# Performance work log

Measured on AMD Instinct MI355X. Metric: run time of the kernel, lower is better.

Reference implementation:

```python
import jax, jax.numpy as jnp
import numpy as np

L, B, D_IN, H, N, NUM_LAYERS = 2048, 16, 64, 512, 64, 4


def setup_inputs() -> dict:
    key = jax.random.key(0)
    ks = jax.random.split(key, 9)
    x = jax.random.normal(ks[0], (L, B, D_IN), dtype=jnp.float32)
    enc_W = jax.random.normal(ks[1], (D_IN, H), dtype=jnp.float32) / np.sqrt(D_IN)
    enc_b = jax.random.normal(ks[2], (H,), dtype=jnp.float32) * 0.01
    # Per-layer S4D parameters, stacked along leading layer axis.
    log_dt = jax.random.uniform(ks[3], (NUM_LAYERS, H), dtype=jnp.float32,
                                minval=np.log(1e-3), maxval=np.log(1e-1))
    log_A_re = jnp.log(0.5 * jnp.ones((NUM_LAYERS, H, N), dtype=jnp.float32))
    A_im = jnp.broadcast_to(np.pi * jnp.arange(N, dtype=jnp.float32),
                            (NUM_LAYERS, H, N)).copy()
    C_re = jax.random.normal(ks[4], (NUM_LAYERS, H, N), dtype=jnp.float32)
    C_im = jax.random.normal(ks[5], (NUM_LAYERS, H, N), dtype=jnp.float32)
    Dskip = jax.random.normal(ks[6], (NUM_LAYERS, H), dtype=jnp.float32)
    return {"x": x, "enc_W": enc_W, "enc_b": enc_b, "log_dt": log_dt,
            "log_A_re": log_A_re, "A_im": A_im, "C_re": C_re, "C_im": C_im,
            "Dskip": Dskip}


def _s4d_layer(u, log_dt, log_A_re, A_im, C_re, C_im, Dskip):
    """u: [L,B,H] real. Diagonal SSM recurrent scan (ZOH discretization)."""
    dt = jnp.exp(log_dt)[:, None]                      # [H,1]
    A = -jnp.exp(log_A_re) + 1j * A_im                 # [H,N] complex, Re<0
    dA = jnp.exp(dt * A)                               # [H,N]
    dB = (dA - 1.0) / A                                # [H,N]
    C = (C_re + 1j * C_im).astype(jnp.complex64)       # [H,N]

    def step(s, u_t):                                  # s:[B,H,N] c64, u_t:[B,H]
        s = dA * s + dB * u_t[..., None]
        y = 2.0 * jnp.einsum('hn,bhn->bh', C, s).real + Dskip * u_t
        return s, y.astype(u_t.dtype)

    s0 = jnp.zeros((u.shape[1], u.shape[2], A.shape[-1]), dtype=jnp.complex64)
    sT, ys = jax.lax.scan(step, s0, u)
    return ys, sT


def reference(x, enc_W, enc_b, log_dt, log_A_re, A_im, C_re, C_im, Dskip):
    # batch_first=False: x is [L,B,D_IN]; torch code transposes to [B,L,·],
    # applies encoder, runs layers, transposes back -> equivalent to keeping
    # time-major [L,B,H] throughout.
    h = x @ enc_W + enc_b                              # [L,B,H]
    states_re, states_im = [], []
    for i in range(NUM_LAYERS):
        h, sT = _s4d_layer(h, log_dt[i], log_A_re[i], A_im[i],
                           C_re[i], C_im[i], Dskip[i])
        states_re.append(sT.real)
        states_im.append(sT.imag)
    return h, jnp.stack(states_re), jnp.stack(states_im)
```

## Files before the change

kernel.cpp:

```cpp
#include <hip/hip_runtime.h>
#include <math.h>

#define L_SEQ 2048
#define B_SZ 16
#define DIN 64
#define H_SZ 512
#define N_ST 64
#define N_LAYERS 4
#define Q_CHUNK 64
#define N_CHUNKS (L_SEQ / Q_CHUNK)
#define GSZ 4
#define N_GROUPS (N_CHUNKS / GSZ)
#define UPAD 2056

typedef _Float16 f16;
typedef _Float16 f16x8 __attribute__((ext_vector_type(8)));
typedef _Float16 f16x4 __attribute__((ext_vector_type(4)));
typedef _Float16 f16x2 __attribute__((ext_vector_type(2)));
typedef float    f32x4 __attribute__((ext_vector_type(4)));
typedef float    f32x2 __attribute__((ext_vector_type(2)));

template <int CTRL>
__device__ __forceinline__ float dpp_add(float x) {
    int s = __builtin_amdgcn_update_dpp(0, __builtin_bit_cast(int, x), CTRL, 0xF, 0xF, false);
    return x + __builtin_bit_cast(float, s);
}
__device__ __forceinline__ float wave_sum_lane63(float x) {
    x = dpp_add<0x111>(x);
    x = dpp_add<0x112>(x);
    x = dpp_add<0x114>(x);
    x = dpp_add<0x118>(x);
    x = dpp_add<0x142>(x);
    x = dpp_add<0x143>(x);
    return x;
}

__device__ __forceinline__ void barrier_lgkm() {
    asm volatile("s_waitcnt lgkmcnt(0)\n\ts_barrier" ::: "memory");
}

__global__ __launch_bounds__(256, 4)
void encoder_mfma_kernel(const float* __restrict__ x, const float* __restrict__ W,
                         const float* __restrict__ bias, f16* __restrict__ out)
{
    __shared__ f16   x_sh[64][72];
    __shared__ f16   w_t[64][72];
    __shared__ float out_sh[64][68];
    __shared__ float b_sh[64];
    const int tid = threadIdx.x;
    const int bid = blockIdx.x;
    const int bb  = bid & 15;
    const int lt  = (bid >> 4) & 31;
    const int ht  = bid >> 9;
    const int l0 = lt * 64, h0 = ht * 64;

#pragma unroll
    for (int i = 0; i < 16; ++i) {
        int idx = tid + i * 256;
        int r = idx >> 6, c = idx & 63;
        x_sh[r][c] = (f16)x[((size_t)(l0 + r) * B_SZ + bb) * DIN + c];
        w_t[c][r]  = (f16)W[(size_t)r * H_SZ + h0 + c];
    }
    if (tid < 64) b_sh[tid] = bias[h0 + tid];
    __syncthreads();

    const int wave = tid >> 6;
    const int lane = tid & 63;
    const int frow = lane & 15;
    const int fk   = (lane >> 4) * 8;
    const int m0   = wave * 16;

    f16x8 a0 = *(const f16x8*)&w_t[m0 + frow][fk];
    f16x8 a1 = *(const f16x8*)&w_t[m0 + frow][fk + 32];
    float bv[4];
#pragma unroll
    for (int j = 0; j < 4; ++j) bv[j] = b_sh[m0 + (lane >> 4) * 4 + j];

#pragma unroll
    for (int nt = 0; nt < 4; ++nt) {
        f16x8 b0 = *(const f16x8*)&x_sh[nt * 16 + frow][fk];
        f16x8 b1 = *(const f16x8*)&x_sh[nt * 16 + frow][fk + 32];
        f32x4 acc = {0.f, 0.f, 0.f, 0.f};
        acc = __builtin_amdgcn_mfma_f32_16x16x32_f16(a0, b0, acc, 0, 0, 0);
        acc = __builtin_amdgcn_mfma_f32_16x16x32_f16(a1, b1, acc, 0, 0, 0);
#pragma unroll
        for (int j = 0; j < 4; ++j)
            out_sh[m0 + (lane >> 4) * 4 + j][nt * 16 + frow] = acc[j] + bv[j];
    }
    __syncthreads();

#pragma unroll
    for (int i = 0; i < 4; ++i) {
        int row = (tid >> 4) + i * 16;
        int c4  = (tid & 15) * 4;
        f32x4 v = *(const f32x4*)&out_sh[row][c4];
        f16x4 o;
#pragma unroll
        for (int k = 0; k < 4; ++k) o[k] = (f16)v[k];
        *(f16x4*)&out[((size_t)(h0 + row) * B_SZ + bb) * L_SEQ + l0 + c4] = o;
    }
}

__global__ __launch_bounds__(1024, 4)
void s4d_fused_kernel(f16* __restrict__ u_io,
                      const float* __restrict__ log_dt, const float* __restrict__ log_A_re,
                      const float* __restrict__ A_im, const float* __restrict__ C_re,
                      const float* __restrict__ C_im, const float* __restrict__ Dskip,
                      float* __restrict__ st_re, float* __restrict__ st_im)
{
    __shared__ f16   A_lds[192][72];
    __shared__ f16   G_lds[64][136];
    __shared__ f16   U_all[16][UPAD];
    __shared__ f16   S_buf[2][GSZ][16][136];
    __shared__ float K_sh[64];
    __shared__ float w_sh[64][2];

    const int tid  = threadIdx.x;
    const int wave = tid >> 6;
    const int lane = tid & 63;
    const int h    = blockIdx.x;
    const int frow = lane & 15;
    const int fq   = lane >> 4;
    const int fk   = fq * 8;

    const bool zrole = (wave < 8);
    const int  ow    = wave - 8;
    const int  orow  = ow & 3;
    const int  ocp   = ow >> 2;

    {
        const f16* ub = u_io + ((size_t)h * B_SZ + wave) * L_SEQ;
#pragma unroll
        for (int p = 0; p < 4; ++p) {
            f16x8 v = *(const f16x8*)&ub[p * 512 + lane * 8];
            *(f16x8*)&U_all[wave][p * 512 + lane * 8] = v;
        }
    }
    f16* yb = u_io + (size_t)h * B_SZ * L_SEQ;

    for (int layer = 0; layer < N_LAYERS; ++layer) {
        const int ph = layer * H_SZ + h;
        const int pn = ph * N_ST + lane;

        float wr = 1.f, wi = 0.f;
        {
            float dt   = expf(log_dt[ph]);
            float Are  = -expf(log_A_re[pn]);
            float Aim  = A_im[pn];
            float mg   = expf(dt * Are);
            float phs  = dt * Aim;
            float dAr  = mg * cosf(phs);
            float dAi  = mg * sinf(phs);
            float invd = 1.0f / (Are * Are + Aim * Aim);
            float nr   = dAr - 1.0f;
            float dBr  = (nr * Are + dAi * Aim) * invd;
            float dBi  = (dAi * Are - nr * Aim) * invd;
            float Cr   = C_re[pn];
            float Ci   = C_im[pn];
            float CBr  = Cr * dBr - Ci * dBi;
            float CBi  = Cr * dBi + Ci * dBr;

            float Pr = 1.f, Pi = 0.f;
            for (int j = 0; j <= 64; ++j) {
                if (j <= 63) {
                    if (wave == 2) {
                        float ks = wave_sum_lane63(2.f * (Pr * CBr - Pi * CBi));
                        if (lane == 63) K_sh[j] = ks;
                    }
                    if (wave == 0) {
                        A_lds[64 + 2 * lane][63 - j]     = (f16)(Pr * dBr - Pi * dBi);
                        A_lds[64 + 2 * lane + 1][63 - j] = (f16)(Pr * dBi + Pi * dBr);
                    }
                }
                if (j >= 1 && wave == 1) {
                    G_lds[j - 1][2 * lane]     = (f16)( 2.f * (Cr * Pr - Ci * Pi));
                    G_lds[j - 1][2 * lane + 1] = (f16)(-2.f * (Cr * Pi + Ci * Pr));
                }
                if (j == 64) { wr = Pr; wi = Pi; }
                float nPr = Pr * dAr - Pi * dAi;
                float nPi = Pr * dAi + Pi * dAr;
                Pr = nPr; Pi = nPi;
            }
        }
        if (wave == 3) { w_sh[lane][0] = wr; w_sh[lane][1] = wi; }
        __syncthreads();
#pragma unroll
        for (int e = tid; e < 64 * 64; e += 1024) {
            int i = e >> 6, j = e & 63;
            A_lds[i][j] = (j <= i) ? (f16)K_sh[i - j] : (f16)0.f;
        }
        __syncthreads();

        const float Dv = Dskip[ph];
        f16x8 aE[2], aT[2], aG[4];
        float s0r = 0.f, s0i = 0.f, s1r = 0.f, s1i = 0.f;
        float war = 0.f, wai = 0.f, wbr = 0.f, wbi = 0.f;
        if (zrole) {
            const int m0 = 64 + wave * 16;
            aE[0] = *(const f16x8*)&A_lds[m0 + frow][fk];
            aE[1] = *(const f16x8*)&A_lds[m0 + frow][fk + 32];
            const int na = wave * 8 + fq * 2;
            war = w_sh[na][0];     wai = w_sh[na][1];
            wbr = w_sh[na + 1][0]; wbi = w_sh[na + 1][1];
        } else {
            const int m0 = orow * 16;
            aT[0] = *(const f16x8*)&A_lds[m0 + frow][fk];
            aT[1] = *(const f16x8*)&A_lds[m0 + frow][fk + 32];
#pragma unroll
            for (int ks = 0; ks < 4; ++ks)
                aG[ks] = *(const f16x8*)&G_lds[m0 + frow][fk + 32 * ks];
        }
        f32x4 yh0 = {0.f,0.f,0.f,0.f}, yh1 = {0.f,0.f,0.f,0.f};

#pragma unroll 2
        for (int g = 0; g <= N_GROUPS + 1; ++g) {
            if (zrole) {
                if (g < N_GROUPS) {
                    const int gb = g & 1;
#pragma unroll
                    for (int j = 0; j < GSZ; ++j) {
                        f16x4 sf; sf[0] = (f16)s0r; sf[1] = (f16)s0i;
                        sf[2] = (f16)s1r; sf[3] = (f16)s1i;
                        *(f16x4*)&S_buf[gb][j][frow][wave * 16 + fq * 4] = sf;
                        const int co = (g * GSZ + j) * 64;
                        f16x8 b0 = *(const f16x8*)&U_all[frow][co + fk];
                        f16x8 b1 = *(const f16x8*)&U_all[frow][co + fk + 32];
                        f32x4 acc = {0.f, 0.f, 0.f, 0.f};
                        acc = __builtin_amdgcn_mfma_f32_16x16x32_f16(aE[0], b0, acc, 0, 0, 0);
                        acc = __builtin_amdgcn_mfma_f32_16x16x32_f16(aE[1], b1, acc, 0, 0, 0);
                        float t0r = war * s0r - wai * s0i + acc[0];
                        float t0i = wai * s0r + war * s0i + acc[1];
                        float t1r = wbr * s1r - wbi * s1i + acc[2];
                        float t1i = wbi * s1r + wbr * s1i + acc[3];
                        s0r = t0r; s0i = t0i; s1r = t1r; s1i = t1i;
                    }
                }
            } else {
                const int t0 = orow * 16 + fq * 4;
                if (layer < N_LAYERS - 1 && g >= 2) {
                    const int c0 = ((g - 2) * GSZ + ocp * 2) * 64;
                    f16x4 o0, o1;
#pragma unroll
                    for (int k = 0; k < 4; ++k) { o0[k] = (f16)yh0[k]; o1[k] = (f16)yh1[k]; }
                    *(f16x4*)&U_all[frow][c0 + t0]      = o0;
                    *(f16x4*)&U_all[frow][c0 + 64 + t0] = o1;
                }
                if (g >= 1 && g <= N_GROUPS) {
                    const int gp = g - 1;
                    const int pb = gp & 1;
#pragma unroll
                    for (int jj = 0; jj < 2; ++jj) {
                        const int j  = ocp * 2 + jj;
                        const int co = (gp * GSZ + j) * 64;
                        f32x4 acc = {0.f, 0.f, 0.f, 0.f};
                        f16x8 b0 = *(const f16x8*)&U_all[frow][co + fk];
                        f16x8 b1 = *(const f16x8*)&U_all[frow][co + fk + 32];
                        acc = __builtin_amdgcn_mfma_f32_16x16x32_f16(aT[0], b0, acc, 0, 0, 0);
                        acc = __builtin_amdgcn_mfma_f32_16x16x32_f16(aT[1], b1, acc, 0, 0, 0);
#pragma unroll
                        for (int ks = 0; ks < 4; ++ks) {
                            f16x8 sv = *(const f16x8*)&S_buf[pb][j][frow][fk + 32 * ks];
                            acc = __builtin_amdgcn_mfma_f32_16x16x32_f16(aG[ks], sv, acc, 0, 0, 0);
                        }
                        f16x4 uf = *(const f16x4*)&U_all[frow][co + t0];
                        f32x4 yv;
#pragma unroll
                        for (int k = 0; k < 4; ++k) yv[k] = acc[k] + Dv * (float)uf[k];
                        if (layer == N_LAYERS - 1) {
                            f16x4 o;
#pragma unroll
                            for (int k = 0; k < 4; ++k) o[k] = (f16)yv[k];
                            *(f16x4*)&yb[(size_t)frow * L_SEQ + co + t0] = o;
                        } else {
                            if (jj == 0) yh0 = yv; else yh1 = yv;
                        }
                    }
                }
            }
            barrier_lgkm();
        }

        if (zrole) {
            const int na = wave * 8 + fq * 2;
            const size_t base = (((size_t)layer * B_SZ + frow) * H_SZ + h) * N_ST + na;
            st_re[base]     = s0r; st_im[base]     = s0i;
            st_re[base + 1] = s1r; st_im[base + 1] = s1i;
        }
        __syncthreads();
    }
}

__global__ __launch_bounds__(256, 4)
void hbl_to_lbh_kernel(const f16* __restrict__ in, float* __restrict__ out)
{
    __shared__ float t_sh[64][65];
    const int tid = threadIdx.x, bid = blockIdx.x;
    const int bb = bid & 15, lt = (bid >> 4) & 31, ht = bid >> 9;
    const int l0 = lt * 64, h0 = ht * 64;
#pragma unroll
    for (int i = 0; i < 4; ++i) {
        int idx = tid + i * 256;
        int hh = idx >> 4, l4 = (idx & 15) * 4;
        f16x4 v = *(const f16x4*)&in[((size_t)(h0 + hh) * B_SZ + bb) * L_SEQ + l0 + l4];
#pragma unroll
        for (int k = 0; k < 4; ++k) t_sh[hh][l4 + k] = (float)v[k];
    }
    __syncthreads();
#pragma unroll
    for (int i = 0; i < 16; ++i) {
        int idx = tid + i * 256;
        int ll = idx >> 6, hh = idx & 63;
        out[((size_t)(l0 + ll) * B_SZ + bb) * H_SZ + h0 + hh] = t_sh[hh][ll];
    }
}

extern "C" void kernel_launch(void* const* d_in, const int* in_sizes, int n_in,
                              void* d_out, int out_size, void* d_ws, size_t ws_size,
                              hipStream_t stream)
{
    const float* x        = (const float*)d_in[0];
    const float* enc_W    = (const float*)d_in[1];
    const float* enc_b    = (const float*)d_in[2];
    const float* log_dt   = (const float*)d_in[3];
    const float* log_A_re = (const float*)d_in[4];
    const float* A_im     = (const float*)d_in[5];
    const float* C_re     = (const float*)d_in[6];
    const float* C_im     = (const float*)d_in[7];
    const float* Dskip    = (const float*)d_in[8];

    float* out_lbh = (float*)d_out;
    float* st_re   = out_lbh + (size_t)L_SEQ * B_SZ * H_SZ;
    float* st_im   = st_re + (size_t)N_LAYERS * B_SZ * H_SZ * N_ST;
    f16*   B0      = (f16*)d_ws;

    encoder_mfma_kernel<<<4096, 256, 0, stream>>>(x, enc_W, enc_b, B0);

    s4d_fused_kernel<<<512, 1024, 0, stream>>>(B0, log_dt, log_A_re, A_im,
                                               C_re, C_im, Dskip, st_re, st_im);

    hbl_to_lbh_kernel<<<4096, 256, 0, stream>>>(B0, out_lbh);
}
```

Before: 263.2 us.

## Rebalance S4D kernel to 768 threads with split real/imag state waves

Shrinks the fused S4D block from 16 to 12 waves. Four state waves now each own 16 state modes, computing real and imaginary parts with separate MFMAs, and eight output waves each produce two 16-row tiles per chunk. The serial 65-step power recurrence used to build the A/G/K tables is split across three segments seeded by repeated squaring. The K kernel is now computed as a small dot product of G with dB rather than a per-step wave reduction. This aims to shorten the per-layer setup and improve the balance between state and output work, at the cost of more registers per wave and a slightly different fp16 rounding path for K.

```diff
diff --git a/kernel.cpp b/kernel.cpp
--- a/kernel.cpp
+++ b/kernel.cpp
@@ -12,27 +12,16 @@
 #define GSZ 4
 #define N_GROUPS (N_CHUNKS / GSZ)
 #define UPAD 2056
+#define NTHR 768
 
 typedef _Float16 f16;
 typedef _Float16 f16x8 __attribute__((ext_vector_type(8)));
 typedef _Float16 f16x4 __attribute__((ext_vector_type(4)));
-typedef _Float16 f16x2 __attribute__((ext_vector_type(2)));
 typedef float    f32x4 __attribute__((ext_vector_type(4)));
-typedef float    f32x2 __attribute__((ext_vector_type(2)));
-
-template <int CTRL>
-__device__ __forceinline__ float dpp_add(float x) {
-    int s = __builtin_amdgcn_update_dpp(0, __builtin_bit_cast(int, x), CTRL, 0xF, 0xF, false);
-    return x + __builtin_bit_cast(float, s);
-}
-__device__ __forceinline__ float wave_sum_lane63(float x) {
-    x = dpp_add<0x111>(x);
-    x = dpp_add<0x112>(x);
-    x = dpp_add<0x114>(x);
-    x = dpp_add<0x118>(x);
-    x = dpp_add<0x142>(x);
-    x = dpp_add<0x143>(x);
-    return x;
+
+struct cx { float r, i; };
+__device__ __forceinline__ cx cmul(cx a, cx b) {
+    return { a.r * b.r - a.i * b.i, a.r * b.i + a.i * b.r };
 }
 
 __device__ __forceinline__ void barrier_lgkm() {
@@ -101,7 +90,7 @@
     }
 }
 
-__global__ __launch_bounds__(1024, 4)
+__global__ __launch_bounds__(NTHR, 3)
 void s4d_fused_kernel(f16* __restrict__ u_io,
                       const float* __restrict__ log_dt, const float* __restrict__ log_A_re,
                       const float* __restrict__ A_im, const float* __restrict__ C_re,
@@ -109,9 +98,10 @@
                       float* __restrict__ st_re, float* __restrict__ st_im)
 {
     __shared__ f16   A_lds[192][72];
-    __shared__ f16   G_lds[64][136];
+    __shared__ f16   G_lds[65][136];
     __shared__ f16   U_all[16][UPAD];
     __shared__ f16   S_buf[2][GSZ][16][136];
+    __shared__ float dBv_sh[128];
     __shared__ float K_sh[64];
     __shared__ float w_sh[64][2];
 
@@ -123,17 +113,11 @@
     const int fq   = lane >> 4;
     const int fk   = fq * 8;
 
-    const bool zrole = (wave < 8);
-    const int  ow    = wave - 8;
-    const int  orow  = ow & 3;
-    const int  ocp   = ow >> 2;
-
     {
-        const f16* ub = u_io + ((size_t)h * B_SZ + wave) * L_SEQ;
-#pragma unroll
-        for (int p = 0; p < 4; ++p) {
-            f16x8 v = *(const f16x8*)&ub[p * 512 + lane * 8];
-            *(f16x8*)&U_all[wave][p * 512 + lane * 8] = v;
+        const f16* ub = u_io + (size_t)h * B_SZ * L_SEQ;
+        for (int u0 = tid; u0 < 16 * 256; u0 += NTHR) {
+            int b = u0 >> 8, cidx = (u0 & 255) * 8;
+            *(f16x8*)&U_all[b][cidx] = *(const f16x8*)&ub[(size_t)b * L_SEQ + cidx];
         }
     }
     f16* yb = u_io + (size_t)h * B_SZ * L_SEQ;
@@ -142,149 +126,179 @@
         const int ph = layer * H_SZ + h;
         const int pn = ph * N_ST + lane;
 
-        float wr = 1.f, wi = 0.f;
         {
             float dt   = expf(log_dt[ph]);
             float Are  = -expf(log_A_re[pn]);
             float Aim  = A_im[pn];
             float mg   = expf(dt * Are);
             float phs  = dt * Aim;
-            float dAr  = mg * cosf(phs);
-            float dAi  = mg * sinf(phs);
+            cx dA1 = { mg * cosf(phs), mg * sinf(phs) };
             float invd = 1.0f / (Are * Are + Aim * Aim);
-            float nr   = dAr - 1.0f;
-            float dBr  = (nr * Are + dAi * Aim) * invd;
-            float dBi  = (dAi * Are - nr * Aim) * invd;
+            float nr   = dA1.r - 1.0f;
+            float dBr  = (nr * Are + dA1.i * Aim) * invd;
+            float dBi  = (dA1.i * Are - nr * Aim) * invd;
             float Cr   = C_re[pn];
             float Ci   = C_im[pn];
-            float CBr  = Cr * dBr - Ci * dBi;
-            float CBi  = Cr * dBi + Ci * dBr;
-
-            float Pr = 1.f, Pi = 0.f;
-            for (int j = 0; j <= 64; ++j) {
-                if (j <= 63) {
-                    if (wave == 2) {
-                        float ks = wave_sum_lane63(2.f * (Pr * CBr - Pi * CBi));
-                        if (lane == 63) K_sh[j] = ks;
-                    }
-                    if (wave == 0) {
-                        A_lds[64 + 2 * lane][63 - j]     = (f16)(Pr * dBr - Pi * dBi);
-                        A_lds[64 + 2 * lane + 1][63 - j] = (f16)(Pr * dBi + Pi * dBr);
-                    }
+            if (wave == 0) { dBv_sh[2 * lane] = dBr; dBv_sh[2 * lane + 1] = dBi; }
+
+            const int role = wave & 3;
+            const int seg  = wave >> 2;
+            cx dA2  = cmul(dA1, dA1);
+            cx dA4  = cmul(dA2, dA2);
+            cx dA8  = cmul(dA4, dA4);
+            cx dA16 = cmul(dA8, dA8);
+            cx P = { 1.f, 0.f };
+            int j0 = 0, jend = 21;
+            if (seg >= 1) { P = cmul(cmul(dA16, dA4), dA1); j0 = 21; jend = 42; }
+            if (seg == 2) { P = cmul(P, P); j0 = 42; jend = (role >= 2) ? 65 : 64; }
+            for (int j = j0; j < jend; ++j) {
+                if (role == 0)      A_lds[64  + lane][63 - j] = (f16)(P.r * dBr - P.i * dBi);
+                else if (role == 1) A_lds[128 + lane][63 - j] = (f16)(P.r * dBi + P.i * dBr);
+                else if (role == 2) G_lds[j][2 * lane]     = (f16)( 2.f * (Cr * P.r - Ci * P.i));
+                else {
+                    G_lds[j][2 * lane + 1] = (f16)(-2.f * (Cr * P.i + Ci * P.r));
+                    if (j == 64) { w_sh[lane][0] = P.r; w_sh[lane][1] = P.i; }
                 }
-                if (j >= 1 && wave == 1) {
-                    G_lds[j - 1][2 * lane]     = (f16)( 2.f * (Cr * Pr - Ci * Pi));
-                    G_lds[j - 1][2 * lane + 1] = (f16)(-2.f * (Cr * Pi + Ci * Pr));
-                }
-                if (j == 64) { wr = Pr; wi = Pi; }
-                float nPr = Pr * dAr - Pi * dAi;
-                float nPi = Pr * dAi + Pi * dAr;
-                Pr = nPr; Pi = nPi;
-            }
-        }
-        if (wave == 3) { w_sh[lane][0] = wr; w_sh[lane][1] = wi; }
-        __syncthreads();
-#pragma unroll
-        for (int e = tid; e < 64 * 64; e += 1024) {
-            int i = e >> 6, j = e & 63;
-            A_lds[i][j] = (j <= i) ? (f16)K_sh[i - j] : (f16)0.f;
-        }
-        __syncthreads();
+                P = cmul(P, dA1);
+            }
+        }
+        barrier_lgkm();
+
+        if (tid < 512) {
+            const int t  = tid >> 3;
+            const int l8 = tid & 7;
+            f16x8 g0 = *(const f16x8*)&G_lds[t][l8 * 16];
+            f16x8 g1 = *(const f16x8*)&G_lds[t][l8 * 16 + 8];
+            f32x4 d0 = *(const f32x4*)&dBv_sh[l8 * 16];
+            f32x4 d1 = *(const f32x4*)&dBv_sh[l8 * 16 + 4];
+            f32x4 d2 = *(const f32x4*)&dBv_sh[l8 * 16 + 8];
+            f32x4 d3 = *(const f32x4*)&dBv_sh[l8 * 16 + 12];
+            float acc = 0.f;
+#pragma unroll
+            for (int k = 0; k < 4; ++k) {
+                acc += (float)g0[k]     * d0[k];
+                acc += (float)g0[k + 4] * d1[k];
+                acc += (float)g1[k]     * d2[k];
+                acc += (float)g1[k + 4] * d3[k];
+            }
+            acc += __shfl_xor(acc, 1);
+            acc += __shfl_xor(acc, 2);
+            acc += __shfl_xor(acc, 4);
+            if (l8 == 0) K_sh[t] = acc;
+        }
+        barrier_lgkm();
+        for (int e = tid; e < 64 * 64; e += NTHR) {
+            int i = e >> 6, jc = e & 63;
+            A_lds[i][jc] = (jc <= i) ? (f16)K_sh[i - jc] : (f16)0.f;
+        }
+        barrier_lgkm();
 
         const float Dv = Dskip[ph];
-        f16x8 aE[2], aT[2], aG[4];
-        float s0r = 0.f, s0i = 0.f, s1r = 0.f, s1i = 0.f;
-        float war = 0.f, wai = 0.f, wbr = 0.f, wbi = 0.f;
-        if (zrole) {
-            const int m0 = 64 + wave * 16;
-            aE[0] = *(const f16x8*)&A_lds[m0 + frow][fk];
-            aE[1] = *(const f16x8*)&A_lds[m0 + frow][fk + 32];
-            const int na = wave * 8 + fq * 2;
-            war = w_sh[na][0];     wai = w_sh[na][1];
-            wbr = w_sh[na + 1][0]; wbi = w_sh[na + 1][1];
+        f16x8 aRe0, aRe1, aIm0, aIm1;
+        f16x8 aT0[2], aT1[2], aG[2][4];
+        float wr4[4], wi4[4];
+        float s_r[4] = {0.f,0.f,0.f,0.f}, s_i[4] = {0.f,0.f,0.f,0.f};
+        if (wave < 4) {
+            const int m0 = 16 * wave;
+            aRe0 = *(const f16x8*)&A_lds[64  + m0 + frow][fk];
+            aRe1 = *(const f16x8*)&A_lds[64  + m0 + frow][fk + 32];
+            aIm0 = *(const f16x8*)&A_lds[128 + m0 + frow][fk];
+            aIm1 = *(const f16x8*)&A_lds[128 + m0 + frow][fk + 32];
+#pragma unroll
+            for (int p = 0; p < 4; ++p) {
+                int n = m0 + fq * 4 + p;
+                wr4[p] = w_sh[n][0]; wi4[p] = w_sh[n][1];
+            }
         } else {
-            const int m0 = orow * 16;
-            aT[0] = *(const f16x8*)&A_lds[m0 + frow][fk];
-            aT[1] = *(const f16x8*)&A_lds[m0 + frow][fk + 32];
-#pragma unroll
-            for (int ks = 0; ks < 4; ++ks)
-                aG[ks] = *(const f16x8*)&G_lds[m0 + frow][fk + 32 * ks];
-        }
-        f32x4 yh0 = {0.f,0.f,0.f,0.f}, yh1 = {0.f,0.f,0.f,0.f};
-
-#pragma unroll 2
+            const int mh = (wave - 4) & 1;
+#pragma unroll
+            for (int mt = 0; mt < 2; ++mt) {
+                const int r0 = 32 * mh + 16 * mt + frow;
+                aT0[mt] = *(const f16x8*)&A_lds[r0][fk];
+                aT1[mt] = *(const f16x8*)&A_lds[r0][fk + 32];
+#pragma unroll
+                for (int k4 = 0; k4 < 4; ++k4)
+                    aG[mt][k4] = *(const f16x8*)&G_lds[1 + r0][fk + 32 * k4];
+            }
+        }
+        f16x4 yh[2];
+
         for (int g = 0; g <= N_GROUPS + 1; ++g) {
-            if (zrole) {
+            if (wave < 4) {
                 if (g < N_GROUPS) {
                     const int gb = g & 1;
 #pragma unroll
                     for (int j = 0; j < GSZ; ++j) {
-                        f16x4 sf; sf[0] = (f16)s0r; sf[1] = (f16)s0i;
-                        sf[2] = (f16)s1r; sf[3] = (f16)s1i;
-                        *(f16x4*)&S_buf[gb][j][frow][wave * 16 + fq * 4] = sf;
+                        f16x8 sf;
+                        sf[0] = (f16)s_r[0]; sf[1] = (f16)s_i[0];
+                        sf[2] = (f16)s_r[1]; sf[3] = (f16)s_i[1];
+                        sf[4] = (f16)s_r[2]; sf[5] = (f16)s_i[2];
+                        sf[6] = (f16)s_r[3]; sf[7] = (f16)s_i[3];
+                        *(f16x8*)&S_buf[gb][j][frow][32 * wave + 8 * fq] = sf;
                         const int co = (g * GSZ + j) * 64;
                         f16x8 b0 = *(const f16x8*)&U_all[frow][co + fk];
                         f16x8 b1 = *(const f16x8*)&U_all[frow][co + fk + 32];
-                        f32x4 acc = {0.f, 0.f, 0.f, 0.f};
-                        acc = __builtin_amdgcn_mfma_f32_16x16x32_f16(aE[0], b0, acc, 0, 0, 0);
-                        acc = __builtin_amdgcn_mfma_f32_16x16x32_f16(aE[1], b1, acc, 0, 0, 0);
-                        float t0r = war * s0r - wai * s0i + acc[0];
-                        float t0i = wai * s0r + war * s0i + acc[1];
-                        float t1r = wbr * s1r - wbi * s1i + acc[2];
-                        float t1i = wbi * s1r + wbr * s1i + acc[3];
-                        s0r = t0r; s0i = t0i; s1r = t1r; s1i = t1i;
+                        f32x4 aR = {0.f,0.f,0.f,0.f}, aI = {0.f,0.f,0.f,0.f};
+                        aR = __builtin_amdgcn_mfma_f32_16x16x32_f16(aRe0, b0, aR, 0, 0, 0);
+                        aR = __builtin_amdgcn_mfma_f32_16x16x32_f16(aRe1, b1, aR, 0, 0, 0);
+                        aI = __builtin_amdgcn_mfma_f32_16x16x32_f16(aIm0, b0, aI, 0, 0, 0);
+                        aI = __builtin_amdgcn_mfma_f32_16x16x32_f16(aIm1, b1, aI, 0, 0, 0);
+#pragma unroll
+                        for (int p = 0; p < 4; ++p) {
+                            float nr2 = wr4[p] * s_r[p] - wi4[p] * s_i[p] + aR[p];
+                            float ni2 = wi4[p] * s_r[p] + wr4[p] * s_i[p] + aI[p];
+                            s_r[p] = nr2; s_i[p] = ni2;
+                        }
                     }
                 }
             } else {
-                const int t0 = orow * 16 + fq * 4;
+                const int ow = wave - 4, jc = ow >> 1, mh = ow & 1;
                 if (layer < N_LAYERS - 1 && g >= 2) {
-                    const int c0 = ((g - 2) * GSZ + ocp * 2) * 64;
-                    f16x4 o0, o1;
-#pragma unroll
-                    for (int k = 0; k < 4; ++k) { o0[k] = (f16)yh0[k]; o1[k] = (f16)yh1[k]; }
-                    *(f16x4*)&U_all[frow][c0 + t0]      = o0;
-                    *(f16x4*)&U_all[frow][c0 + 64 + t0] = o1;
+                    const int co2 = ((g - 2) * GSZ + jc) * 64;
+                    *(f16x4*)&U_all[frow][co2 + 32 * mh + fq * 4]      = yh[0];
+                    *(f16x4*)&U_all[frow][co2 + 32 * mh + 16 + fq * 4] = yh[1];
                 }
                 if (g >= 1 && g <= N_GROUPS) {
-                    const int gp = g - 1;
-                    const int pb = gp & 1;
-#pragma unroll
-                    for (int jj = 0; jj < 2; ++jj) {
-                        const int j  = ocp * 2 + jj;
-                        const int co = (gp * GSZ + j) * 64;
-                        f32x4 acc = {0.f, 0.f, 0.f, 0.f};
-                        f16x8 b0 = *(const f16x8*)&U_all[frow][co + fk];
-                        f16x8 b1 = *(const f16x8*)&U_all[frow][co + fk + 32];
-                        acc = __builtin_amdgcn_mfma_f32_16x16x32_f16(aT[0], b0, acc, 0, 0, 0);
-                        acc = __builtin_amdgcn_mfma_f32_16x16x32_f16(aT[1], b1, acc, 0, 0, 0);
-#pragma unroll
-                        for (int ks = 0; ks < 4; ++ks) {
-                            f16x8 sv = *(const f16x8*)&S_buf[pb][j][frow][fk + 32 * ks];
-                            acc = __builtin_amdgcn_mfma_f32_16x16x32_f16(aG[ks], sv, acc, 0, 0, 0);
-                        }
+                    const int gp = g - 1, pb = gp & 1;
+                    const int co = (gp * GSZ + jc) * 64;
+                    f16x8 b0 = *(const f16x8*)&U_all[frow][co + fk];
+                    f16x8 b1 = *(const f16x8*)&U_all[frow][co + fk + 32];
+                    f16x8 sv0 = *(const f16x8*)&S_buf[pb][jc][frow][fk];
+                    f16x8 sv1 = *(const f16x8*)&S_buf[pb][jc][frow][fk + 32];
+                    f16x8 sv2 = *(const f16x8*)&S_buf[pb][jc][frow][fk + 64];
+                    f16x8 sv3 = *(const f16x8*)&S_buf[pb][jc][frow][fk + 96];
+#pragma unroll
+                    for (int mt = 0; mt < 2; ++mt) {
+                        f32x4 acc = {0.f,0.f,0.f,0.f};
+                        acc = __builtin_amdgcn_mfma_f32_16x16x32_f16(aT0[mt], b0, acc, 0, 0, 0);
+                        acc = __builtin_amdgcn_mfma_f32_16x16x32_f16(aT1[mt], b1, acc, 0, 0, 0);
+                        acc = __builtin_amdgcn_mfma_f32_16x16x32_f16(aG[mt][0], sv0, acc, 0, 0, 0);
+                        acc = __builtin_amdgcn_mfma_f32_16x16x32_f16(aG[mt][1], sv1, acc, 0, 0, 0);
+                        acc = __builtin_amdgcn_mfma_f32_16x16x32_f16(aG[mt][2], sv2, acc, 0, 0, 0);
+                        acc = __builtin_amdgcn_mfma_f32_16x16x32_f16(aG[mt][3], sv3, acc, 0, 0, 0);
+                        const int t0 = 32 * mh + 16 * mt + fq * 4;
                         f16x4 uf = *(const f16x4*)&U_all[frow][co + t0];
-                        f32x4 yv;
-#pragma unroll
-                        for (int k = 0; k < 4; ++k) yv[k] = acc[k] + Dv * (float)uf[k];
-                        if (layer == N_LAYERS - 1) {
-                            f16x4 o;
-#pragma unroll
-                            for (int k = 0; k < 4; ++k) o[k] = (f16)yv[k];
+                        f16x4 o;
+#pragma unroll
+                        for (int k = 0; k < 4; ++k) o[k] = (f16)(acc[k] + Dv * (float)uf[k]);
+                        if (layer == N_LAYERS - 1)
                             *(f16x4*)&yb[(size_t)frow * L_SEQ + co + t0] = o;
-                        } else {
-                            if (jj == 0) yh0 = yv; else yh1 = yv;
-                        }
+                        else
+                            yh[mt] = o;
                     }
                 }
             }
             barrier_lgkm();
         }
 
-        if (zrole) {
-            const int na = wave * 8 + fq * 2;
-            const size_t base = (((size_t)layer * B_SZ + frow) * H_SZ + h) * N_ST + na;
-            st_re[base]     = s0r; st_im[base]     = s0i;
-            st_re[base + 1] = s1r; st_im[base + 1] = s1i;
+        if (wave < 4) {
+#pragma unroll
+            for (int p = 0; p < 4; ++p) {
+                int n = 16 * wave + 4 * fq + p;
+                size_t base = (((size_t)layer * B_SZ + frow) * H_SZ + h) * N_ST + n;
+                st_re[base] = s_r[p];
+                st_im[base] = s_i[p];
+            }
         }
         __syncthreads();
     }
@@ -335,7 +349,7 @@
 
     encoder_mfma_kernel<<<4096, 256, 0, stream>>>(x, enc_W, enc_b, B0);
 
-    s4d_fused_kernel<<<512, 1024, 0, stream>>>(B0, log_dt, log_A_re, A_im,
+    s4d_fused_kernel<<<512, NTHR, 0, stream>>>(B0, log_dt, log_A_re, A_im,
                                                C_re, C_im, Dskip, st_re, st_im);
 
     hbl_to_lbh_kernel<<<4096, 256, 0, stream>>>(B0, out_lbh);
```

Result: faster. 243.3 us (-7.6%).
